# Kernel tuning notes

Hardware: AMD Instinct MI355X
Metric: run time of the kernel (lower is better)

The kernel has to match this reference:

```python
import jax, jax.numpy as jnp
import numpy as np

B, Q, K, H = 16, 512, 512, 64
DQ, DK, DV = 256, 256, 256
MASK_VAL = -1000000.0


def setup_inputs() -> dict:
    key = jax.random.key(0)
    ks = jax.random.split(key, 7)
    queries = jax.random.normal(ks[0], (B, Q, DQ), dtype=jnp.float32)
    keys = jax.random.normal(ks[1], (B, K, DK), dtype=jnp.float32)
    values = jax.random.normal(ks[2], (B, K, DV), dtype=jnp.float32)
    valid_lens = jax.random.randint(ks[3], (B,), 1, K + 1).astype(jnp.int32)
    # learned params (nn.Linear, bias=False): weight shape [out, in]
    Wq = jax.random.normal(ks[4], (H, DQ), dtype=jnp.float32) / np.sqrt(DQ)
    Wk = jax.random.normal(ks[5], (H, DK), dtype=jnp.float32) / np.sqrt(DK)
    wv = jax.random.normal(ks[6], (H,), dtype=jnp.float32) / np.sqrt(H)
    return {"queries": queries, "keys": keys, "values": values,
            "valid_lens": valid_lens, "Wq": Wq, "Wk": Wk, "wv": wv}


def reference(queries, keys, values, valid_lens, Wq, Wk, wv):
    q = jnp.einsum('bqd,hd->bqh', queries, Wq)          # [B,Q,H]
    k = jnp.einsum('bkd,hd->bkh', keys, Wk)             # [B,K,H]
    feats = jnp.tanh(q[:, :, None, :] + k[:, None, :, :])  # [B,Q,K,H]
    scores = jnp.einsum('bqkh,h->bqk', feats, wv)       # [B,Q,K]
    kmask = jnp.arange(K)[None, None, :] < valid_lens[:, None, None]
    scores = jnp.where(kmask, scores, MASK_VAL)
    attn = jax.nn.softmax(scores, axis=-1)              # [B,Q,K]
    return jnp.einsum('bqk,bkv->bqv', attn, values)     # [B,Q,DV]
```

## Files before the change

### kernel.cpp

```cpp
#include <hip/hip_runtime.h>
#include <math.h>

#if defined(__has_builtin)
#  if __has_builtin(__builtin_amdgcn_exp2f)
#    define EXP2F(x) __builtin_amdgcn_exp2f(x)
#  endif
#  if __has_builtin(__builtin_amdgcn_rcpf)
#    define RCPF(x) __builtin_amdgcn_rcpf(x)
#  endif
#endif
#ifndef EXP2F
#  define EXP2F(x) exp2f(x)
#endif
#ifndef RCPF
#  define RCPF(x) (1.0f/(x))
#endif

static constexpr int Bn = 16, QN = 512, KN = 512, Hn = 64, DV = 256, DIN = 256;
static constexpr int TQ = 4;
static constexpr float TWO_LOG2E = 2.8853900817779268f;
static constexpr float LOG2E     = 1.4426950408889634f;

typedef __attribute__((ext_vector_type(8))) short short8;
typedef __attribute__((ext_vector_type(4))) float f32x4;

__device__ __forceinline__ short f2bf(float x) {
  unsigned u = __builtin_bit_cast(unsigned, x);
  u += 0x7FFF + ((u >> 16) & 1);
  return (short)(u >> 16);
}
__device__ __forceinline__ float bf2f(short h) {
  return __builtin_bit_cast(float, ((unsigned)(unsigned short)h) << 16);
}
__device__ __forceinline__ float rdlane(float v, int l) {
  return __builtin_bit_cast(float,
      __builtin_amdgcn_readlane(__builtin_bit_cast(int, v), l));
}

__global__ __launch_bounds__(256) void proj_mfma(
    const float* __restrict__ queries, const float* __restrict__ keys,
    const float* __restrict__ Wq, const float* __restrict__ Wk,
    const float* __restrict__ wv,
    float* __restrict__ qT, float* __restrict__ ekT, float* __restrict__ wv2)
{
  __shared__ float tr[4][16][20];
  int t = threadIdx.x;
  int lane = t & 63, wid = t >> 6;
  if (blockIdx.x == 0 && t < Hn) wv2[t] = 2.0f * wv[t];
  bool is_k = blockIdx.x >= 512;
  int trow = (blockIdx.x & 511) * 16;
  const float* X = is_k ? keys : queries;
  const float* W = is_k ? Wk : Wq;
  float* dT = is_k ? ekT : qT;
  int mr = lane & 15, quad = lane >> 4;
  const float* xp = X + (size_t)(trow + mr) * DIN + quad * 8;
  const float* wp = W + (size_t)(wid * 16 + mr) * DIN + quad * 8;

  f32x4 acc = (f32x4){0.f, 0.f, 0.f, 0.f};
  #pragma unroll
  for (int kc = 0; kc < 8; ++kc) {
    float4 a0 = *(const float4*)(xp + kc * 32);
    float4 a1 = *(const float4*)(xp + kc * 32 + 4);
    float4 b0 = *(const float4*)(wp + kc * 32);
    float4 b1 = *(const float4*)(wp + kc * 32 + 4);
    float av[8] = {a0.x, a0.y, a0.z, a0.w, a1.x, a1.y, a1.z, a1.w};
    float bv[8] = {b0.x, b0.y, b0.z, b0.w, b1.x, b1.y, b1.z, b1.w};
    short8 ah, al, bh, bl;
    #pragma unroll
    for (int j = 0; j < 8; ++j) {
      ah[j] = f2bf(av[j]);
      al[j] = f2bf(av[j] - bf2f(ah[j]));
      bh[j] = f2bf(bv[j]);
      bl[j] = f2bf(bv[j] - bf2f(bh[j]));
    }
    acc = __builtin_amdgcn_mfma_f32_16x16x32_bf16(al, bh, acc, 0, 0, 0);
    acc = __builtin_amdgcn_mfma_f32_16x16x32_bf16(ah, bl, acc, 0, 0, 0);
    acc = __builtin_amdgcn_mfma_f32_16x16x32_bf16(ah, bh, acc, 0, 0, 0);
  }
  #pragma unroll
  for (int reg = 0; reg < 4; ++reg)
    tr[wid][mr][quad * 4 + reg] = EXP2F(acc[reg] * TWO_LOG2E);
  int b = trow >> 9, rr = trow & 511;
  #pragma unroll
  for (int hp = 0; hp < 4; ++hp) {
    int h_l = hp * 4 + quad, r_l = mr;
    dT[((size_t)b * Hn + wid * 16 + h_l) * 512 + rr + r_l] = tr[wid][h_l][r_l];
  }
}

__global__ __launch_bounds__(512) void attn_kernel(
    const float* __restrict__ qT,
    const float* __restrict__ ekT,
    const float* __restrict__ values,
    const int*   __restrict__ valid_lens,
    const float* __restrict__ wv2,
    float* __restrict__ out)
{
  __shared__ __align__(16) float pt[KN][TQ];
  __shared__ __align__(16) float pacc[TQ][DV];
  __shared__ float wsum[8][TQ];
  __shared__ float inv_s[TQ];
  __shared__ int srank[Bn];

  int t = threadIdx.x;
  int lane = t & 63, wave = t >> 6;

  if (t < Bn) {
    int Lb = valid_lens[t];
    int r = 0;
    #pragma unroll
    for (int b2 = 0; b2 < Bn; ++b2) {
      int L2 = valid_lens[b2];
      r += (L2 > Lb || (L2 == Lb && b2 < t)) ? 1 : 0;
    }
    srank[r] = t;
  }
  __syncthreads();

  int rank = blockIdx.x >> 7;
  int b = __builtin_amdgcn_readfirstlane(srank[rank]);
  int L = __builtin_amdgcn_readfirstlane(valid_lens[b]);
  int q0 = (blockIdx.x & 127) * TQ;

  float S = 0.f;
  #pragma unroll
  for (int h = 0; h < Hn; ++h) S += wv2[h];
  S *= 0.5f;

  {
    int k = t;
    float p[TQ];
    if (k < L) {
      float sc[TQ];
      #pragma unroll
      for (int r = 0; r < TQ; ++r) sc[r] = S;
      const float* kp = ekT + (size_t)b * Hn * KN + k;
      const float* qb = qT  + (size_t)b * Hn * QN + q0;
      float ekv[8];
      #pragma unroll
      for (int j = 0; j < 8; ++j)
        ekv[j] = kp[(size_t)j * KN];
      #pragma unroll
      for (int h0 = 0; h0 < Hn; h0 += 8) {
        float ekn[8];
        if (h0 + 8 < Hn) {
          #pragma unroll
          for (int j = 0; j < 8; ++j)
            ekn[j] = kp[(size_t)(h0 + 8 + j) * KN];
        }
        #pragma unroll
        for (int jp = 0; jp < 4; ++jp) {
          int ha = h0 + 2 * jp;
          float wa = wv2[ha], wb = wv2[ha + 1];
          float4 qa = *(const float4*)(qb + (size_t)ha * QN);
          float4 qc = *(const float4*)(qb + (size_t)(ha + 1) * QN);
          float eka = ekv[2 * jp], ekb = ekv[2 * jp + 1];
          float da, db, num;
          da = qa.x * eka + 1.0f; db = qc.x * ekb + 1.0f;
          num = wa * db + wb * da; sc[0] -= num * RCPF(da * db);
          da = qa.y * eka + 1.0f; db = qc.y * ekb + 1.0f;
          num = wa * db + wb * da; sc[1] -= num * RCPF(da * db);
          da = qa.z * eka + 1.0f; db = qc.z * ekb + 1.0f;
          num = wa * db + wb * da; sc[2] -= num * RCPF(da * db);
          da = qa.w * eka + 1.0f; db = qc.w * ekb + 1.0f;
          num = wa * db + wb * da; sc[3] -= num * RCPF(da * db);
        }
        if (h0 + 8 < Hn) {
          #pragma unroll
          for (int j = 0; j < 8; ++j) ekv[j] = ekn[j];
        }
      }
      #pragma unroll
      for (int r = 0; r < TQ; ++r) p[r] = EXP2F(sc[r] * LOG2E);
      *(float4*)&pt[k][0] = make_float4(p[0], p[1], p[2], p[3]);
    } else {
      #pragma unroll
      for (int r = 0; r < TQ; ++r) p[r] = 0.f;
    }
    #pragma unroll
    for (int r = 0; r < TQ; ++r) {
      float s = p[r];
      #pragma unroll
      for (int off = 32; off > 0; off >>= 1) s += __shfl_xor(s, off, 64);
      if (lane == r) wsum[wave][r] = s;
    }
  }
  __syncthreads();
  if (t < TQ) {
    float s = 0.f;
    #pragma unroll
    for (int w = 0; w < 8; ++w) s += wsum[w][t];
    inv_s[t] = 1.0f / s;
  }

  int c = t & (DV - 1), half = t >> 8;
  int mid = L >> 1;
  int k0 = half ? mid : 0;
  int k1 = half ? L : mid;
  float acc[TQ] = {0.f, 0.f, 0.f, 0.f};
  const float* vb = values + (size_t)b * KN * DV + c;
  int kb = k0;
  for (; kb + 64 <= k1; kb += 64) {
    float4 pj = *(const float4*)&pt[kb + lane][0];
    const float* vp = vb + (size_t)kb * DV;
    float vv[8];
    #pragma unroll
    for (int j = 0; j < 8; ++j) vv[j] = vp[(size_t)j * DV];
    #pragma unroll
    for (int g = 0; g < 8; ++g) {
      float vn[8];
      if (g < 7) {
        #pragma unroll
        for (int j = 0; j < 8; ++j)
          vn[j] = vp[(size_t)(g * 8 + 8 + j) * DV];
      }
      #pragma unroll
      for (int j = 0; j < 8; ++j) {
        int l = g * 8 + j;
        float p0 = rdlane(pj.x, l), p1 = rdlane(pj.y, l);
        float p2 = rdlane(pj.z, l), p3 = rdlane(pj.w, l);
        acc[0] += p0 * vv[j]; acc[1] += p1 * vv[j];
        acc[2] += p2 * vv[j]; acc[3] += p3 * vv[j];
      }
      if (g < 7) {
        #pragma unroll
        for (int j = 0; j < 8; ++j) vv[j] = vn[j];
      }
    }
  }
  #pragma unroll 2
  for (int k = kb; k < k1; ++k) {
    float val = vb[(size_t)k * DV];
    float4 pa = *(const float4*)&pt[k][0];
    acc[0] += pa.x * val; acc[1] += pa.y * val;
    acc[2] += pa.z * val; acc[3] += pa.w * val;
  }
  if (half) {
    #pragma unroll
    for (int r = 0; r < TQ; ++r) pacc[r][c] = acc[r];
  }
  __syncthreads();
  if (!half) {
    float* ob = out + (size_t)(b * QN + q0) * DV + c;
    #pragma unroll
    for (int r = 0; r < TQ; ++r)
      ob[(size_t)r * DV] = (acc[r] + pacc[r][c]) * inv_s[r];
  }
}

extern "C" void kernel_launch(void* const* d_in, const int* in_sizes, int n_in,
                              void* d_out, int out_size, void* d_ws, size_t ws_size,
                              hipStream_t stream) {
  const float* queries    = (const float*)d_in[0];
  const float* keys       = (const float*)d_in[1];
  const float* values     = (const float*)d_in[2];
  const int*   valid_lens = (const int*)d_in[3];
  const float* Wq         = (const float*)d_in[4];
  const float* Wk         = (const float*)d_in[5];
  const float* wv         = (const float*)d_in[6];
  float* out = (float*)d_out;

  char* ws = (char*)d_ws;
  float* qT  = (float*)ws;
  float* ekT = qT + (size_t)Bn * Hn * QN;
  float* wv2 = ekT + (size_t)Bn * Hn * KN;

  proj_mfma<<<1024, 256, 0, stream>>>(queries, keys, Wq, Wk, wv, qT, ekT, wv2);
  attn_kernel<<<Bn * (QN / TQ), 512, 0, stream>>>(qT, ekT, values,
                                                  valid_lens, wv2, out);
}
```

Baseline: 172.3 us.

## Double query tile per block, reorder batch schedule, read probabilities from LDS

Each attention block now handles 8 queries instead of 4, halving the block count. Every loaded key projection and value element is reused across twice as many queries. The P·V loop drops the readlane broadcast and reads probabilities from LDS as two float4 loads per key, with a padded row stride of 12. Blocks are now assigned to batches in a snake order over the length ranking to balance load. The cost is more registers per thread and fewer blocks, which may reduce occupancy.

```diff
diff --git a/kernel.cpp b/kernel.cpp
--- a/kernel.cpp
+++ b/kernel.cpp
@@ -17,7 +17,7 @@
 #endif
 
 static constexpr int Bn = 16, QN = 512, KN = 512, Hn = 64, DV = 256, DIN = 256;
-static constexpr int TQ = 4;
+static constexpr int TQ = 8;
 static constexpr float TWO_LOG2E = 2.8853900817779268f;
 static constexpr float LOG2E     = 1.4426950408889634f;
 
@@ -31,10 +31,6 @@
 }
 __device__ __forceinline__ float bf2f(short h) {
   return __builtin_bit_cast(float, ((unsigned)(unsigned short)h) << 16);
-}
-__device__ __forceinline__ float rdlane(float v, int l) {
-  return __builtin_bit_cast(float,
-      __builtin_amdgcn_readlane(__builtin_bit_cast(int, v), l));
 }
 
 __global__ __launch_bounds__(256) void proj_mfma(
@@ -96,7 +92,7 @@
     const float* __restrict__ wv2,
     float* __restrict__ out)
 {
-  __shared__ __align__(16) float pt[KN][TQ];
+  __shared__ __align__(16) float pt[KN][12];
   __shared__ __align__(16) float pacc[TQ][DV];
   __shared__ float wsum[8][TQ];
   __shared__ float inv_s[TQ];
@@ -117,10 +113,12 @@
   }
   __syncthreads();
 
-  int rank = blockIdx.x >> 7;
-  int b = __builtin_amdgcn_readfirstlane(srank[rank]);
+  int slot = blockIdx.x >> 6;
+  int gq = slot >> 2, iq = slot & 3;
+  int jr = (gq == 0) ? iq : (gq == 1) ? 7 - iq : (gq == 2) ? 8 + iq : 15 - iq;
+  int b = __builtin_amdgcn_readfirstlane(srank[jr]);
   int L = __builtin_amdgcn_readfirstlane(valid_lens[b]);
-  int q0 = (blockIdx.x & 127) * TQ;
+  int q0 = (blockIdx.x & 63) * TQ;
 
   float S = 0.f;
   #pragma unroll
@@ -152,18 +150,28 @@
         for (int jp = 0; jp < 4; ++jp) {
           int ha = h0 + 2 * jp;
           float wa = wv2[ha], wb = wv2[ha + 1];
-          float4 qa = *(const float4*)(qb + (size_t)ha * QN);
-          float4 qc = *(const float4*)(qb + (size_t)(ha + 1) * QN);
+          float4 qa0 = *(const float4*)(qb + (size_t)ha * QN);
+          float4 qa1 = *(const float4*)(qb + (size_t)ha * QN + 4);
+          float4 qc0 = *(const float4*)(qb + (size_t)(ha + 1) * QN);
+          float4 qc1 = *(const float4*)(qb + (size_t)(ha + 1) * QN + 4);
           float eka = ekv[2 * jp], ekb = ekv[2 * jp + 1];
           float da, db, num;
-          da = qa.x * eka + 1.0f; db = qc.x * ekb + 1.0f;
+          da = qa0.x * eka + 1.0f; db = qc0.x * ekb + 1.0f;
           num = wa * db + wb * da; sc[0] -= num * RCPF(da * db);
-          da = qa.y * eka + 1.0f; db = qc.y * ekb + 1.0f;
+          da = qa0.y * eka + 1.0f; db = qc0.y * ekb + 1.0f;
           num = wa * db + wb * da; sc[1] -= num * RCPF(da * db);
-          da = qa.z * eka + 1.0f; db = qc.z * ekb + 1.0f;
+          da = qa0.z * eka + 1.0f; db = qc0.z * ekb + 1.0f;
           num = wa * db + wb * da; sc[2] -= num * RCPF(da * db);
-          da = qa.w * eka + 1.0f; db = qc.w * ekb + 1.0f;
+          da = qa0.w * eka + 1.0f; db = qc0.w * ekb + 1.0f;
           num = wa * db + wb * da; sc[3] -= num * RCPF(da * db);
+          da = qa1.x * eka + 1.0f; db = qc1.x * ekb + 1.0f;
+          num = wa * db + wb * da; sc[4] -= num * RCPF(da * db);
+          da = qa1.y * eka + 1.0f; db = qc1.y * ekb + 1.0f;
+          num = wa * db + wb * da; sc[5] -= num * RCPF(da * db);
+          da = qa1.z * eka + 1.0f; db = qc1.z * ekb + 1.0f;
+          num = wa * db + wb * da; sc[6] -= num * RCPF(da * db);
+          da = qa1.w * eka + 1.0f; db = qc1.w * ekb + 1.0f;
+          num = wa * db + wb * da; sc[7] -= num * RCPF(da * db);
         }
         if (h0 + 8 < Hn) {
           #pragma unroll
@@ -173,6 +181,7 @@
       #pragma unroll
       for (int r = 0; r < TQ; ++r) p[r] = EXP2F(sc[r] * LOG2E);
       *(float4*)&pt[k][0] = make_float4(p[0], p[1], p[2], p[3]);
+      *(float4*)&pt[k][4] = make_float4(p[4], p[5], p[6], p[7]);
     } else {
       #pragma unroll
       for (int r = 0; r < TQ; ++r) p[r] = 0.f;
@@ -197,43 +206,57 @@
   int mid = L >> 1;
   int k0 = half ? mid : 0;
   int k1 = half ? L : mid;
-  float acc[TQ] = {0.f, 0.f, 0.f, 0.f};
+  float acc[TQ];
+  #pragma unroll
+  for (int r = 0; r < TQ; ++r) acc[r] = 0.f;
   const float* vb = values + (size_t)b * KN * DV + c;
+  int n8 = (k1 - k0) >> 3;
   int kb = k0;
-  for (; kb + 64 <= k1; kb += 64) {
-    float4 pj = *(const float4*)&pt[kb + lane][0];
-    const float* vp = vb + (size_t)kb * DV;
+  if (n8 > 0) {
     float vv[8];
     #pragma unroll
-    for (int j = 0; j < 8; ++j) vv[j] = vp[(size_t)j * DV];
-    #pragma unroll
-    for (int g = 0; g < 8; ++g) {
+    for (int j = 0; j < 8; ++j) vv[j] = vb[(size_t)(k0 + j) * DV];
+    for (int g = 0; g < n8 - 1; ++g) {
+      int kc = k0 + g * 8;
       float vn[8];
-      if (g < 7) {
-        #pragma unroll
-        for (int j = 0; j < 8; ++j)
-          vn[j] = vp[(size_t)(g * 8 + 8 + j) * DV];
+      #pragma unroll
+      for (int j = 0; j < 8; ++j)
+        vn[j] = vb[(size_t)(kc + 8 + j) * DV];
+      #pragma unroll
+      for (int j = 0; j < 8; ++j) {
+        float4 pa = *(const float4*)&pt[kc + j][0];
+        float4 pb = *(const float4*)&pt[kc + j][4];
+        float val = vv[j];
+        acc[0] += pa.x * val; acc[1] += pa.y * val;
+        acc[2] += pa.z * val; acc[3] += pa.w * val;
+        acc[4] += pb.x * val; acc[5] += pb.y * val;
+        acc[6] += pb.z * val; acc[7] += pb.w * val;
       }
       #pragma unroll
-      for (int j = 0; j < 8; ++j) {
-        int l = g * 8 + j;
-        float p0 = rdlane(pj.x, l), p1 = rdlane(pj.y, l);
-        float p2 = rdlane(pj.z, l), p3 = rdlane(pj.w, l);
-        acc[0] += p0 * vv[j]; acc[1] += p1 * vv[j];
-        acc[2] += p2 * vv[j]; acc[3] += p3 * vv[j];
-      }
-      if (g < 7) {
-        #pragma unroll
-        for (int j = 0; j < 8; ++j) vv[j] = vn[j];
-      }
-    }
+      for (int j = 0; j < 8; ++j) vv[j] = vn[j];
+    }
+    int kc = k0 + (n8 - 1) * 8;
+    #pragma unroll
+    for (int j = 0; j < 8; ++j) {
+      float4 pa = *(const float4*)&pt[kc + j][0];
+      float4 pb = *(const float4*)&pt[kc + j][4];
+      float val = vv[j];
+      acc[0] += pa.x * val; acc[1] += pa.y * val;
+      acc[2] += pa.z * val; acc[3] += pa.w * val;
+      acc[4] += pb.x * val; acc[5] += pb.y * val;
+      acc[6] += pb.z * val; acc[7] += pb.w * val;
+    }
+    kb = k0 + n8 * 8;
   }
   #pragma unroll 2
-  for (int k = kb; k < k1; ++k) {
-    float val = vb[(size_t)k * DV];
-    float4 pa = *(const float4*)&pt[k][0];
+  for (; kb < k1; ++kb) {
+    float val = vb[(size_t)kb * DV];
+    float4 pa = *(const float4*)&pt[kb][0];
+    float4 pb = *(const float4*)&pt[kb][4];
     acc[0] += pa.x * val; acc[1] += pa.y * val;
     acc[2] += pa.z * val; acc[3] += pa.w * val;
+    acc[4] += pb.x * val; acc[5] += pb.y * val;
+    acc[6] += pb.z * val; acc[7] += pb.w * val;
   }
   if (half) {
     #pragma unroll
```

Measured after the change: 181.2 us. 1.05x slower.
